# Kernel tuning notes

Measured on AMD Instinct MI355X. Metric: run time of the kernel, lower is better.

Reference implementation:

```python
import jax, jax.numpy as jnp
import numpy as np

PRIMES = [250007, 250013, 250027, 250031, 250037, 250043, 250049, 250051]
OFFSETS = np.concatenate([[0], np.cumsum(PRIMES)[:-1]]).astype(np.int64)  # [8]
TOTAL_ROWS = int(np.sum(PRIMES))
D_HEAD = 128          # embedding_dim_per_head
E_DIM = 8 * D_HEAD    # total_embedding_dim = 1024
H_DIM = 2560          # hidden_dim
KSIZE = 4             # causal depthwise conv kernel
EPS = 1e-6


def rmsnorm(x, g):
    # torch.nn.RMSNorm: x / sqrt(mean(x^2) + eps) * weight
    return x * jax.lax.rsqrt(jnp.mean(x * x, axis=-1, keepdims=True) + EPS) * g


def setup_inputs() -> dict:
    key = jax.random.key(0)
    ks = jax.random.split(key, 10)
    B, L = 4, 4096
    return {
        "hidden_states": jax.random.normal(ks[0], (B, L, H_DIM), jnp.float32),
        "engram_hash_indices": jax.random.randint(ks[1], (B, L, 8), 0, 250007, jnp.int64),
        "emb_table": jax.random.normal(ks[2], (TOTAL_ROWS, D_HEAD), jnp.float32) * 0.02,
        "w_v": jax.random.normal(ks[3], (H_DIM, E_DIM), jnp.float32) * 0.02,
        "w_k": jax.random.normal(ks[4], (H_DIM, E_DIM), jnp.float32) * 0.02,
        "g_h": jnp.ones((H_DIM,), jnp.float32),
        "g_k": jnp.ones((H_DIM,), jnp.float32),
        "g_v": jnp.ones((H_DIM,), jnp.float32),
        # paper zero-inits the conv; use small random weights so the conv path is exercised
        "conv_w": jax.random.normal(ks[5], (H_DIM, KSIZE), jnp.float32) * 0.02,
        "conv_b": jax.random.normal(ks[6], (H_DIM,), jnp.float32) * 0.02,
    }


def reference(hidden_states, engram_hash_indices, emb_table, w_v, w_k, g_h, g_k, g_v, conv_w, conv_b):
    B, L, H = hidden_states.shape
    # multi-head hash embedding retrieval
    idx = engram_hash_indices + jnp.asarray(OFFSETS)            # [B,L,8]
    e_t = emb_table[idx].reshape(B, L, E_DIM)                    # gather + concat heads
    # value / key projections (Linear, no bias)
    v_t = jnp.einsum('ble,he->blh', e_t, w_v)                    # [B,L,H]
    k_t = jnp.einsum('ble,he->blh', e_t, w_k)
    # context-aware gating
    h_n = rmsnorm(hidden_states, g_h)
    k_n = rmsnorm(k_t, g_k)
    dot = jnp.sum(h_n * k_n, axis=-1) / jnp.sqrt(jnp.float32(H))  # [B,L]
    stable = jnp.sqrt(jnp.maximum(jnp.abs(dot), 1e-6)) * jnp.sign(dot)
    alpha = jax.nn.sigmoid(stable)                               # [B,L]
    v_tilde = alpha[..., None] * v_t                             # [B,L,H]
    v_n = rmsnorm(v_tilde, g_v)
    # causal depthwise conv1d (left pad K-1) + SiLU
    x_pad = jnp.pad(v_n, ((0, 0), (KSIZE - 1, 0), (0, 0)))       # [B,L+3,H]
    conv = sum(conv_w[:, j] * x_pad[:, j:j + L, :] for j in range(KSIZE)) + conv_b
    y = jax.nn.silu(conv) + v_tilde
    return hidden_states + y
```

## Files before the change

kernel.cpp:

```cpp
#include <hip/hip_runtime.h>
#include <cstddef>
#include <cstdint>

typedef __bf16 bf16;
typedef __bf16 bf16x4 __attribute__((ext_vector_type(4)));
typedef __bf16 bf16x8 __attribute__((ext_vector_type(8)));
typedef float f32x4 __attribute__((ext_vector_type(4)));

#define AS1C(p) ((const __attribute__((address_space(1))) void*)(p))
#define AS3(p)  ((__attribute__((address_space(3))) void*)(p))

#define MROWS 16384
#define HDIM 2560
#define EDIM 1024
#define LSEQ 4096

static __device__ const int kHeadOff[8] = {0, 250007, 500020, 750047,
                                           1000078, 1250115, 1500158, 1750207};

__global__ __launch_bounds__(256) void k_gather(const int* __restrict__ hidx,
                                                const float* __restrict__ emb,
                                                bf16* __restrict__ E) {
  const int t = threadIdx.x;
  const int m = blockIdx.x * 2 + (t >> 7);
  const int tt = t & 127;
  const int head = tt >> 4;
  const int e8 = (tt & 15) * 8;
  const int rid = hidx[m * 8 + head] + kHeadOff[head];
  const float4 v0 = *(const float4*)(emb + (size_t)rid * 128 + e8);
  const float4 v1 = *(const float4*)(emb + (size_t)rid * 128 + e8 + 4);
  bf16x8 o;
  o[0] = (bf16)v0.x; o[1] = (bf16)v0.y; o[2] = (bf16)v0.z; o[3] = (bf16)v0.w;
  o[4] = (bf16)v1.x; o[5] = (bf16)v1.y; o[6] = (bf16)v1.z; o[7] = (bf16)v1.w;
  *(bf16x8*)(E + (size_t)m * EDIM + head * 128 + e8) = o;
}

__global__ __launch_bounds__(256) void k_cvt2(const float* __restrict__ s0,
                                              bf16* __restrict__ d0,
                                              const float* __restrict__ s1,
                                              bf16* __restrict__ d1) {
  int b = blockIdx.x;
  const float* src = s0;
  bf16* dst = d0;
  if (b >= 1280) { b -= 1280; src = s1; dst = d1; }
  const int i = (b * 256 + threadIdx.x) * 8;
  float4 a = *(const float4*)(src + i);
  float4 c = *(const float4*)(src + i + 4);
  bf16x8 o;
  o[0] = (bf16)a.x; o[1] = (bf16)a.y; o[2] = (bf16)a.z; o[3] = (bf16)a.w;
  o[4] = (bf16)c.x; o[5] = (bf16)c.y; o[6] = (bf16)c.z; o[7] = (bf16)c.w;
  *(bf16x8*)(dst + i) = o;
}

__device__ __forceinline__ float red16(float v) {
  v += __shfl_xor(v, 1);
  v += __shfl_xor(v, 2);
  v += __shfl_xor(v, 4);
  v += __shfl_xor(v, 8);
  return v;
}


#define LDSB 24576

__global__ __launch_bounds__(512, 4) void k_gemm(const bf16* __restrict__ A,
                                                 const bf16* __restrict__ Wv,
                                                 const bf16* __restrict__ Wk,
                                                 const float* __restrict__ hidden,
                                                 const float* __restrict__ g_h,
                                                 const float* __restrict__ g_k,
                                                 bf16* __restrict__ Vt,
                                                 float* __restrict__ S) {
  __shared__ __attribute__((aligned(16))) char ldsc[2 * LDSB];
  const int tid = threadIdx.x;
  const int wid = tid >> 6, lane = tid & 63;
  const int wm = wid >> 1, wn = wid & 1;
  const int r16 = lane & 15, khalf = lane >> 4;

  const int w = blockIdx.x;
  const int xcd = w & 7;
  const int r_ = w >> 3;
  const int gx = r_ >> 3;
  const int y = xcd * 8 + (r_ & 7);
  const int m0 = y * 256;
  const bool isV = (gx < 20);
  const int n0 = (isV ? gx : gx - 20) * 128;
  const bf16* Wp = isV ? Wv : Wk;

  const int sw = ((r16 >> 1) & 3) << 4;
  const int c0 = (khalf * 16) ^ sw;
  const int aRd = (wm * 64 + r16) * 64 + c0;
  const int bRd = 16384 + (wn * 64 + r16) * 64 + c0;

  const int srow = tid >> 2;
  const int scol = (((tid & 3) ^ ((tid >> 3) & 3))) * 8;
  const bf16* pA0 = A + (size_t)(m0 + srow) * EDIM + scol;
  const bf16* pA1 = pA0 + (size_t)128 * EDIM;
  const bf16* pB = Wp + (size_t)(n0 + srow) * EDIM + scol;
  const int ldsW = wid * 1024;

  f32x4 acc[4][4] = {};

#define STAGE(BUFO, KT) do {                                                   \
    __builtin_amdgcn_global_load_lds(AS1C(pA0 + (KT) * 32),                    \
        AS3(ldsc + (BUFO) + ldsW), 16, 0, 0);                                  \
    __builtin_amdgcn_global_load_lds(AS1C(pA1 + (KT) * 32),                    \
        AS3(ldsc + (BUFO) + 8192 + ldsW), 16, 0, 0);                           \
    __builtin_amdgcn_global_load_lds(AS1C(pB + (KT) * 32),                     \
        AS3(ldsc + (BUFO) + 16384 + ldsW), 16, 0, 0);                          \
    __builtin_amdgcn_sched_barrier(0);                                         \
  } while (0)

#define PHASE_CORE(BUFO) do {                                                  \
    bf16x8 aF[4], bF[4];                                                       \
    _Pragma("unroll") for (int mi = 0; mi < 4; ++mi)                           \
      aF[mi] = *(const bf16x8*)(ldsc + (BUFO) + aRd + mi * 1024);              \
    _Pragma("unroll") for (int nj = 0; nj < 4; ++nj)                           \
      bF[nj] = *(const bf16x8*)(ldsc + (BUFO) + bRd + nj * 1024);              \
    __builtin_amdgcn_s_setprio(1);                                             \
    _Pragma("unroll") for (int nj = 0; nj < 4; ++nj)                           \
      _Pragma("unroll") for (int mi = 0; mi < 4; ++mi)                         \
        acc[mi][nj] = __builtin_amdgcn_mfma_f32_16x16x32_bf16(                 \
            aF[mi], bF[nj], acc[mi][nj], 0, 0, 0);                             \
    __builtin_amdgcn_s_setprio(0);                                             \
    asm volatile("s_waitcnt lgkmcnt(0)" ::: "memory");                         \
    __builtin_amdgcn_s_barrier();                                              \
  } while (0)

#define BEGIN_PHASE3() do {                                                    \
    asm volatile("s_waitcnt vmcnt(3)" ::: "memory");                           \
    __builtin_amdgcn_s_barrier();                                              \
    asm volatile("" ::: "memory");                                             \
  } while (0)

#define BEGIN_PHASE0() do {                                                    \
    asm volatile("s_waitcnt vmcnt(0)" ::: "memory");                           \
    __builtin_amdgcn_s_barrier();                                              \
    asm volatile("" ::: "memory");                                             \
  } while (0)

  STAGE(0, 0);
  STAGE(LDSB, 1);

  for (int p = 0; p < 30; p += 2) {
    BEGIN_PHASE3();
    PHASE_CORE(0);
    STAGE(0, p + 2);
    BEGIN_PHASE3();
    PHASE_CORE(LDSB);
    STAGE(LDSB, p + 3);
  }
  BEGIN_PHASE3();
  PHASE_CORE(0);
  BEGIN_PHASE0();
  PHASE_CORE(LDSB);

  float* P = (float*)ldsc;
  if (isV) {
#pragma unroll
    for (int mi = 0; mi < 4; ++mi) {
#pragma unroll
      for (int nj = 0; nj < 4; ++nj) {
        const int col = n0 + wn * 64 + nj * 16 + r16;
#pragma unroll
        for (int r = 0; r < 4; ++r) {
          const int row = m0 + wm * 64 + mi * 16 + khalf * 4 + r;
          Vt[(size_t)row * HDIM + col] = (bf16)acc[mi][nj][r];
        }
      }
#pragma unroll
      for (int r = 0; r < 4; ++r) {
        float p = 0.f;
#pragma unroll
        for (int nj = 0; nj < 4; ++nj) p += acc[mi][nj][r] * acc[mi][nj][r];
        p = red16(p);
        if (r16 == 0) {
          const int rl = wm * 64 + mi * 16 + khalf * 4 + r;
          P[wn * 256 + rl] = p;
        }
      }
    }
    __syncthreads();
    if (tid < 256) {
      const float s = P[tid] + P[256 + tid];
      atomicAdd(&S[(size_t)(m0 + tid) * 4 + 3], s);
    }
  } else {
    float ghk[4];
#pragma unroll
    for (int nj = 0; nj < 4; ++nj) {
      const int col = n0 + wn * 64 + nj * 16 + r16;
      ghk[nj] = g_h[col] * g_k[col];
    }
#pragma unroll
    for (int mi = 0; mi < 4; ++mi) {
#pragma unroll
      for (int r = 0; r < 4; ++r) {
        const int row = m0 + wm * 64 + mi * 16 + khalf * 4 + r;
        float p1 = 0.f, p2 = 0.f, p3 = 0.f;
#pragma unroll
        for (int nj = 0; nj < 4; ++nj) {
          const int col = n0 + wn * 64 + nj * 16 + r16;
          const float k = acc[mi][nj][r];
          const float h = hidden[(size_t)row * HDIM + col];
          p1 += h * h;
          p2 += h * ghk[nj] * k;
          p3 += k * k;
        }
        p1 = red16(p1); p2 = red16(p2); p3 = red16(p3);
        if (r16 == 0) {
          const int rl = wm * 64 + mi * 16 + khalf * 4 + r;
          float* Pr = P + (wn * 256 + rl) * 3;
          Pr[0] = p1; Pr[1] = p2; Pr[2] = p3;
        }
      }
    }
    __syncthreads();
    for (int j = tid; j < 768; j += 512) {
      const int rl = j / 3, c = j % 3;
      const float s = P[j] + P[768 + j];
      atomicAdd(&S[(size_t)(m0 + rl) * 4 + c], s);
    }
  }
#undef STAGE
#undef PHASE_CORE
#undef BEGIN_PHASE3
#undef BEGIN_PHASE0
}

__global__ __launch_bounds__(256) void k_scal(const float* __restrict__ S,
                                              float* __restrict__ AB) {
  const int m = blockIdx.x * 256 + threadIdx.x;
  const float s1 = S[(size_t)m * 4 + 0];
  const float s2 = S[(size_t)m * 4 + 1];
  const float s3 = S[(size_t)m * 4 + 2];
  const float s4 = S[(size_t)m * 4 + 3];
  const float inv_h = rsqrtf(s1 * (1.f / HDIM) + 1e-6f);
  const float inv_k = rsqrtf(s3 * (1.f / HDIM) + 1e-6f);
  const float dot = s2 * inv_h * inv_k * 0.019764235f;
  float st = sqrtf(fmaxf(fabsf(dot), 1e-6f));
  st = (dot < 0.f) ? -st : st;
  if (dot == 0.f) st = 0.f;
  const float alpha = 1.f / (1.f + __expf(-st));
  const float inv_v = rsqrtf(alpha * alpha * s4 * (1.f / HDIM) + 1e-6f);
  AB[(size_t)m * 2 + 0] = alpha;
  AB[(size_t)m * 2 + 1] = alpha * inv_v;
}

__global__ __launch_bounds__(320) void k_fuse(const float* __restrict__ hidden,
                                              const bf16* __restrict__ Vt,
                                              const float* __restrict__ AB,
                                              const float* __restrict__ g_v,
                                              const float* __restrict__ conv_w,
                                              const float* __restrict__ conv_b,
                                              float* __restrict__ out) {
  const int mbase = blockIdx.x * 8;
  const int l0 = mbase & (LSEQ - 1);
  const int t = threadIdx.x;
  const int h0 = t * 8;

  float gv[8], cb[8];
  *(float4*)&gv[0] = *(const float4*)(g_v + h0);
  *(float4*)&gv[4] = *(const float4*)(g_v + h0 + 4);
  *(float4*)&cb[0] = *(const float4*)(conv_b + h0);
  *(float4*)&cb[4] = *(const float4*)(conv_b + h0 + 4);
  float4 cw[8];
#pragma unroll
  for (int i = 0; i < 8; ++i)
    cw[i] = *(const float4*)(conv_w + (size_t)(h0 + i) * 4);

  float win[4][8];
#pragma unroll
  for (int jj = 0; jj < 4; ++jj)
#pragma unroll
    for (int i = 0; i < 8; ++i) win[jj][i] = 0.f;

#pragma unroll
  for (int j = 0; j < 11; ++j) {
    const int lj = l0 - 3 + j;
    const int m = mbase - 3 + j;
    float vtl[8];
    if (lj >= 0) {
      const float alpha = AB[(size_t)m * 2 + 0];
      const float av = AB[(size_t)m * 2 + 1];
      const bf16x8 v = *(const bf16x8*)(Vt + (size_t)m * HDIM + h0);
#pragma unroll
      for (int i = 0; i < 8; ++i) {
        const float vt = (float)v[i];
        vtl[i] = alpha * vt;
        win[j & 3][i] = av * vt * gv[i];
      }
    } else {
#pragma unroll
      for (int i = 0; i < 8; ++i) { win[j & 3][i] = 0.f; vtl[i] = 0.f; }
    }
    if (j >= 3) {
      const int R = mbase + j - 3;
      const size_t base = (size_t)R * HDIM + h0;
      float hx[8];
      *(float4*)&hx[0] = *(const float4*)(hidden + base);
      *(float4*)&hx[4] = *(const float4*)(hidden + base + 4);
      float o[8];
#pragma unroll
      for (int i = 0; i < 8; ++i) {
        float c = cb[i];
        c += ((const float*)&cw[i])[0] * win[(j - 3) & 3][i];
        c += ((const float*)&cw[i])[1] * win[(j - 2) & 3][i];
        c += ((const float*)&cw[i])[2] * win[(j - 1) & 3][i];
        c += ((const float*)&cw[i])[3] * win[j & 3][i];
        const float y = c / (1.f + __expf(-c));
        o[i] = hx[i] + y + vtl[i];
      }
      *(float4*)(out + base) = *(float4*)&o[0];
      *(float4*)(out + base + 4) = *(float4*)&o[4];
    }
  }
}

extern "C" void kernel_launch(void* const* d_in, const int* in_sizes, int n_in,
                              void* d_out, int out_size, void* d_ws,
                              size_t ws_size, hipStream_t stream) {
  const float* hidden = (const float*)d_in[0];
  const int* hashidx = (const int*)d_in[1];
  const float* emb = (const float*)d_in[2];
  const float* w_v = (const float*)d_in[3];
  const float* w_k = (const float*)d_in[4];
  const float* g_h = (const float*)d_in[5];
  const float* g_k = (const float*)d_in[6];
  const float* g_v = (const float*)d_in[7];
  const float* conv_w = (const float*)d_in[8];
  const float* conv_b = (const float*)d_in[9];
  float* out = (float*)d_out;

  char* w = (char*)d_ws;
  bf16* e16 = (bf16*)w;  w += (size_t)MROWS * EDIM * 2;
  bf16* wv16 = (bf16*)w; w += (size_t)HDIM * EDIM * 2;
  bf16* wk16 = (bf16*)w; w += (size_t)HDIM * EDIM * 2;
  bf16* vt16 = (bf16*)w; w += (size_t)MROWS * HDIM * 2;
  float* S = (float*)w;  w += (size_t)MROWS * 4 * 4;
  float* AB = (float*)w; w += (size_t)MROWS * 2 * 4;

  hipMemsetAsync(S, 0, (size_t)MROWS * 4 * 4, stream);
  k_gather<<<MROWS / 2, 256, 0, stream>>>(hashidx, emb, e16);
  k_cvt2<<<2560, 256, 0, stream>>>(w_v, wv16, w_k, wk16);
  k_gemm<<<dim3(2560), 512, 0, stream>>>(e16, wv16, wk16, hidden, g_h, g_k,
                                         vt16, S);
  k_scal<<<MROWS / 256, 256, 0, stream>>>(S, AB);
  k_fuse<<<MROWS / 8, 320, 0, stream>>>(hidden, vt16, AB, g_v, conv_w, conv_b,
                                        out);
}
```

Baseline: 325.4 us.

## Pre-pack gathered A in MFMA fragment layout and load A directly into registers

The gather kernel now writes the bf16 embedding matrix in a pre-swizzled fragment-major layout, so each lane of a GEMM wave can read its MFMA A-operand with one contiguous 16-byte global load. The GEMM stops staging A through LDS: it double-buffers A fragments in registers (aX/aY) and only stages the weight tile B through LDS, which cuts LDS use from 48KB to 16KB and removes the A LDS writes and reads. The cost is A reuse across the two wn waves, which now comes from L2/cache instead of LDS, and extra register pressure. The gather kernel also changes its thread mapping, with each thread now converting a 64-element half-row per head.

Result: slower. 335.8 us (+3.2%).

```diff
diff --git a/kernel.cpp b/kernel.cpp
--- a/kernel.cpp
+++ b/kernel.cpp
@@ -20,19 +20,26 @@
 
 __global__ __launch_bounds__(256) void k_gather(const int* __restrict__ hidx,
                                                 const float* __restrict__ emb,
-                                                bf16* __restrict__ E) {
+                                                bf16* __restrict__ Ap) {
   const int t = threadIdx.x;
-  const int m = blockIdx.x * 2 + (t >> 7);
-  const int tt = t & 127;
-  const int head = tt >> 4;
-  const int e8 = (tt & 15) * 8;
-  const int rid = hidx[m * 8 + head] + kHeadOff[head];
-  const float4 v0 = *(const float4*)(emb + (size_t)rid * 128 + e8);
-  const float4 v1 = *(const float4*)(emb + (size_t)rid * 128 + e8 + 4);
-  bf16x8 o;
-  o[0] = (bf16)v0.x; o[1] = (bf16)v0.y; o[2] = (bf16)v0.z; o[3] = (bf16)v0.w;
-  o[4] = (bf16)v1.x; o[5] = (bf16)v1.y; o[6] = (bf16)v1.z; o[7] = (bf16)v1.w;
-  *(bf16x8*)(E + (size_t)m * EDIM + head * 128 + e8) = o;
+  const int m16 = t & 15, c = t >> 4;
+  const int mbase = blockIdx.x * 16;
+  const int head = c >> 1;
+  const int rid = hidx[(mbase + m16) * 8 + head] + kHeadOff[head];
+  const float* src = emb + (size_t)rid * 128 + (c & 1) * 64;
+  char* dstbase = (char*)Ap + ((size_t)blockIdx.x * 32 + c * 2) * 1024;
+#pragma unroll
+  for (int j64 = 0; j64 < 2; ++j64) {
+#pragma unroll
+    for (int q = 0; q < 4; ++q) {
+      const float4 v0 = *(const float4*)(src + j64 * 32 + q * 8);
+      const float4 v1 = *(const float4*)(src + j64 * 32 + q * 8 + 4);
+      bf16x8 o;
+      o[0] = (bf16)v0.x; o[1] = (bf16)v0.y; o[2] = (bf16)v0.z; o[3] = (bf16)v0.w;
+      o[4] = (bf16)v1.x; o[5] = (bf16)v1.y; o[6] = (bf16)v1.z; o[7] = (bf16)v1.w;
+      *(bf16x8*)(dstbase + j64 * 1024 + (m16 + 16 * q) * 16) = o;
+    }
+  }
 }
 
 __global__ __launch_bounds__(256) void k_cvt2(const float* __restrict__ s0,
@@ -61,9 +68,7 @@
 }
 
 
-#define LDSB 24576
-
-__global__ __launch_bounds__(512, 4) void k_gemm(const bf16* __restrict__ A,
+__global__ __launch_bounds__(512, 4) void k_gemm(const bf16* __restrict__ Af,
                                                  const bf16* __restrict__ Wv,
                                                  const bf16* __restrict__ Wk,
                                                  const float* __restrict__ hidden,
@@ -71,7 +76,7 @@
                                                  const float* __restrict__ g_k,
                                                  bf16* __restrict__ Vt,
                                                  float* __restrict__ S) {
-  __shared__ __attribute__((aligned(16))) char ldsc[2 * LDSB];
+  __shared__ __attribute__((aligned(16))) char ldsc[16384];
   const int tid = threadIdx.x;
   const int wid = tid >> 6, lane = tid & 63;
   const int wm = wid >> 1, wn = wid & 1;
@@ -87,73 +92,58 @@
   const int n0 = (isV ? gx : gx - 20) * 128;
   const bf16* Wp = isV ? Wv : Wk;
 
+  const char* aF0 = (const char*)Af + ((size_t)(y * 16 + wm * 4) * 32) * 1024 +
+                    lane * 16;
   const int sw = ((r16 >> 1) & 3) << 4;
   const int c0 = (khalf * 16) ^ sw;
-  const int aRd = (wm * 64 + r16) * 64 + c0;
-  const int bRd = 16384 + (wn * 64 + r16) * 64 + c0;
+  const int bRd = (wn * 64 + r16) * 64 + c0;
 
   const int srow = tid >> 2;
   const int scol = (((tid & 3) ^ ((tid >> 3) & 3))) * 8;
-  const bf16* pA0 = A + (size_t)(m0 + srow) * EDIM + scol;
-  const bf16* pA1 = pA0 + (size_t)128 * EDIM;
   const bf16* pB = Wp + (size_t)(n0 + srow) * EDIM + scol;
-  const int ldsW = wid * 1024;
 
   f32x4 acc[4][4] = {};
-
-#define STAGE(BUFO, KT) do {                                                   \
-    __builtin_amdgcn_global_load_lds(AS1C(pA0 + (KT) * 32),                    \
-        AS3(ldsc + (BUFO) + ldsW), 16, 0, 0);                                  \
-    __builtin_amdgcn_global_load_lds(AS1C(pA1 + (KT) * 32),                    \
-        AS3(ldsc + (BUFO) + 8192 + ldsW), 16, 0, 0);                           \
+  bf16x8 aX[4], aY[4], bF[4];
+
+#define STAGEB(BUFO, KT) do {                                                  \
     __builtin_amdgcn_global_load_lds(AS1C(pB + (KT) * 32),                     \
-        AS3(ldsc + (BUFO) + 16384 + ldsW), 16, 0, 0);                          \
+        AS3(ldsc + (BUFO) + tid * 16), 16, 0, 0);                              \
     __builtin_amdgcn_sched_barrier(0);                                         \
   } while (0)
 
-#define PHASE_CORE(BUFO) do {                                                  \
-    bf16x8 aF[4], bF[4];                                                       \
+#define LOADA(DST, KT) do {                                                    \
     _Pragma("unroll") for (int mi = 0; mi < 4; ++mi)                           \
-      aF[mi] = *(const bf16x8*)(ldsc + (BUFO) + aRd + mi * 1024);              \
+      DST[mi] = *(const bf16x8*)(aF0 + ((size_t)mi * 32 + (KT)) * 1024);       \
+  } while (0)
+
+#define PHASE(BUFO, ACUR, ANEXT, KT, LD_A, ST_B, VMC) do {                     \
+    asm volatile("s_waitcnt vmcnt(" #VMC ")" ::: "memory");                    \
+    __builtin_amdgcn_s_barrier();                                              \
+    asm volatile("" ::: "memory");                                             \
+    if (LD_A) LOADA(ANEXT, (KT) + 1);                                          \
     _Pragma("unroll") for (int nj = 0; nj < 4; ++nj)                           \
       bF[nj] = *(const bf16x8*)(ldsc + (BUFO) + bRd + nj * 1024);              \
     __builtin_amdgcn_s_setprio(1);                                             \
     _Pragma("unroll") for (int nj = 0; nj < 4; ++nj)                           \
       _Pragma("unroll") for (int mi = 0; mi < 4; ++mi)                         \
         acc[mi][nj] = __builtin_amdgcn_mfma_f32_16x16x32_bf16(                 \
-            aF[mi], bF[nj], acc[mi][nj], 0, 0, 0);                             \
+            ACUR[mi], bF[nj], acc[mi][nj], 0, 0, 0);                           \
     __builtin_amdgcn_s_setprio(0);                                             \
     asm volatile("s_waitcnt lgkmcnt(0)" ::: "memory");                         \
     __builtin_amdgcn_s_barrier();                                              \
+    if (ST_B) STAGEB(BUFO, (KT) + 2);                                          \
   } while (0)
 
-#define BEGIN_PHASE3() do {                                                    \
-    asm volatile("s_waitcnt vmcnt(3)" ::: "memory");                           \
-    __builtin_amdgcn_s_barrier();                                              \
-    asm volatile("" ::: "memory");                                             \
-  } while (0)
-
-#define BEGIN_PHASE0() do {                                                    \
-    asm volatile("s_waitcnt vmcnt(0)" ::: "memory");                           \
-    __builtin_amdgcn_s_barrier();                                              \
-    asm volatile("" ::: "memory");                                             \
-  } while (0)
-
-  STAGE(0, 0);
-  STAGE(LDSB, 1);
+  STAGEB(0, 0);
+  STAGEB(8192, 1);
+  LOADA(aX, 0);
 
   for (int p = 0; p < 30; p += 2) {
-    BEGIN_PHASE3();
-    PHASE_CORE(0);
-    STAGE(0, p + 2);
-    BEGIN_PHASE3();
-    PHASE_CORE(LDSB);
-    STAGE(LDSB, p + 3);
+    PHASE(0, aX, aY, p, true, true, 5);
+    PHASE(8192, aY, aX, p + 1, true, true, 5);
   }
-  BEGIN_PHASE3();
-  PHASE_CORE(0);
-  BEGIN_PHASE0();
-  PHASE_CORE(LDSB);
+  PHASE(0, aX, aY, 30, true, false, 5);
+  PHASE(8192, aY, aX, 31, false, false, 4);
 
   float* P = (float*)ldsc;
   if (isV) {
@@ -222,10 +212,9 @@
       atomicAdd(&S[(size_t)(m0 + rl) * 4 + c], s);
     }
   }
-#undef STAGE
-#undef PHASE_CORE
-#undef BEGIN_PHASE3
-#undef BEGIN_PHASE0
+#undef STAGEB
+#undef LOADA
+#undef PHASE
 }
 
 __global__ __launch_bounds__(256) void k_scal(const float* __restrict__ S,
@@ -333,7 +322,7 @@
   float* out = (float*)d_out;
 
   char* w = (char*)d_ws;
-  bf16* e16 = (bf16*)w;  w += (size_t)MROWS * EDIM * 2;
+  bf16* a16 = (bf16*)w;  w += (size_t)MROWS * EDIM * 2;
   bf16* wv16 = (bf16*)w; w += (size_t)HDIM * EDIM * 2;
   bf16* wk16 = (bf16*)w; w += (size_t)HDIM * EDIM * 2;
   bf16* vt16 = (bf16*)w; w += (size_t)MROWS * HDIM * 2;
@@ -341,9 +330,9 @@
   float* AB = (float*)w; w += (size_t)MROWS * 2 * 4;
 
   hipMemsetAsync(S, 0, (size_t)MROWS * 4 * 4, stream);
-  k_gather<<<MROWS / 2, 256, 0, stream>>>(hashidx, emb, e16);
+  k_gather<<<MROWS / 16, 256, 0, stream>>>(hashidx, emb, a16);
   k_cvt2<<<2560, 256, 0, stream>>>(w_v, wv16, w_k, wk16);
-  k_gemm<<<dim3(2560), 512, 0, stream>>>(e16, wv16, wk16, hidden, g_h, g_k,
+  k_gemm<<<dim3(2560), 512, 0, stream>>>(a16, wv16, wk16, hidden, g_h, g_k,
                                          vt16, S);
   k_scal<<<MROWS / 256, 256, 0, stream>>>(S, AB);
   k_fuse<<<MROWS / 8, 320, 0, stream>>>(hidden, vt16, AB, g_v, conv_w, conv_b,
```

## Triple-buffer GEMM LDS pipeline and fold scalar kernel into fuse kernel

Applied to the files above, without the earlier changes.

The GEMM main loop moves from double to triple buffering in LDS, issuing the next tile's global-to-LDS loads at the start of each phase. The goal is to cut the stall between the barrier and the next load. Separately, the per-row gating scalars (alpha and the value-norm scale) are now computed inline in the fuse kernel from S, which removes the k_scal launch and the AB buffer. The cost is larger LDS use (72KB per block), which may reduce occupancy, and redundant per-row scalar math in each fuse thread.

New measurement: 329.7 us. No clear change (+1.3%).

```diff
diff --git a/kernel.cpp b/kernel.cpp
--- a/kernel.cpp
+++ b/kernel.cpp
@@ -71,7 +71,7 @@
                                                  const float* __restrict__ g_k,
                                                  bf16* __restrict__ Vt,
                                                  float* __restrict__ S) {
-  __shared__ __attribute__((aligned(16))) char ldsc[2 * LDSB];
+  __shared__ __attribute__((aligned(16))) char ldsc[3 * LDSB];
   const int tid = threadIdx.x;
   const int wid = tid >> 6, lane = tid & 63;
   const int wm = wid >> 1, wn = wid & 1;
@@ -111,7 +111,8 @@
     __builtin_amdgcn_sched_barrier(0);                                         \
   } while (0)
 
-#define PHASE_CORE(BUFO) do {                                                  \
+#define PHASE(BUFO, STBUF, KT, ST, VMW) do {                                   \
+    if (ST) STAGE(STBUF, (KT) + 2);                                            \
     bf16x8 aF[4], bF[4];                                                       \
     _Pragma("unroll") for (int mi = 0; mi < 4; ++mi)                           \
       aF[mi] = *(const bf16x8*)(ldsc + (BUFO) + aRd + mi * 1024);              \
@@ -123,37 +124,22 @@
         acc[mi][nj] = __builtin_amdgcn_mfma_f32_16x16x32_bf16(                 \
             aF[mi], bF[nj], acc[mi][nj], 0, 0, 0);                             \
     __builtin_amdgcn_s_setprio(0);                                             \
-    asm volatile("s_waitcnt lgkmcnt(0)" ::: "memory");                         \
+    asm volatile("s_waitcnt " VMW " lgkmcnt(0)" ::: "memory");                 \
     __builtin_amdgcn_s_barrier();                                              \
   } while (0)
 
-#define BEGIN_PHASE3() do {                                                    \
-    asm volatile("s_waitcnt vmcnt(3)" ::: "memory");                           \
-    __builtin_amdgcn_s_barrier();                                              \
-    asm volatile("" ::: "memory");                                             \
-  } while (0)
-
-#define BEGIN_PHASE0() do {                                                    \
-    asm volatile("s_waitcnt vmcnt(0)" ::: "memory");                           \
-    __builtin_amdgcn_s_barrier();                                              \
-    asm volatile("" ::: "memory");                                             \
-  } while (0)
-
   STAGE(0, 0);
   STAGE(LDSB, 1);
-
-  for (int p = 0; p < 30; p += 2) {
-    BEGIN_PHASE3();
-    PHASE_CORE(0);
-    STAGE(0, p + 2);
-    BEGIN_PHASE3();
-    PHASE_CORE(LDSB);
-    STAGE(LDSB, p + 3);
+  asm volatile("s_waitcnt vmcnt(3)" ::: "memory");
+  __builtin_amdgcn_s_barrier();
+
+  for (int p = 0; p < 30; p += 3) {
+    PHASE(0,        2 * LDSB, p,     true, "vmcnt(3)");
+    PHASE(LDSB,     0,        p + 1, true, "vmcnt(3)");
+    PHASE(2 * LDSB, LDSB,     p + 2, true, "vmcnt(3)");
   }
-  BEGIN_PHASE3();
-  PHASE_CORE(0);
-  BEGIN_PHASE0();
-  PHASE_CORE(LDSB);
+  PHASE(0, 0, 30, false, "vmcnt(0)");
+  PHASE(LDSB, 0, 31, false, "");
 
   float* P = (float*)ldsc;
   if (isV) {
@@ -223,33 +209,25 @@
     }
   }
 #undef STAGE
-#undef PHASE_CORE
-#undef BEGIN_PHASE3
-#undef BEGIN_PHASE0
-}
-
-__global__ __launch_bounds__(256) void k_scal(const float* __restrict__ S,
-                                              float* __restrict__ AB) {
-  const int m = blockIdx.x * 256 + threadIdx.x;
-  const float s1 = S[(size_t)m * 4 + 0];
-  const float s2 = S[(size_t)m * 4 + 1];
-  const float s3 = S[(size_t)m * 4 + 2];
-  const float s4 = S[(size_t)m * 4 + 3];
-  const float inv_h = rsqrtf(s1 * (1.f / HDIM) + 1e-6f);
-  const float inv_k = rsqrtf(s3 * (1.f / HDIM) + 1e-6f);
-  const float dot = s2 * inv_h * inv_k * 0.019764235f;
+#undef PHASE
+}
+
+__device__ __forceinline__ void row_scal(const float* __restrict__ S, int m,
+                                         float& alpha, float& av) {
+  const float4 s = *(const float4*)(S + (size_t)m * 4);
+  const float inv_h = rsqrtf(s.x * (1.f / HDIM) + 1e-6f);
+  const float inv_k = rsqrtf(s.z * (1.f / HDIM) + 1e-6f);
+  const float dot = s.y * inv_h * inv_k * 0.019764235f;
   float st = sqrtf(fmaxf(fabsf(dot), 1e-6f));
   st = (dot < 0.f) ? -st : st;
   if (dot == 0.f) st = 0.f;
-  const float alpha = 1.f / (1.f + __expf(-st));
-  const float inv_v = rsqrtf(alpha * alpha * s4 * (1.f / HDIM) + 1e-6f);
-  AB[(size_t)m * 2 + 0] = alpha;
-  AB[(size_t)m * 2 + 1] = alpha * inv_v;
+  alpha = 1.f / (1.f + __expf(-st));
+  av = alpha * rsqrtf(alpha * alpha * s.w * (1.f / HDIM) + 1e-6f);
 }
 
 __global__ __launch_bounds__(320) void k_fuse(const float* __restrict__ hidden,
                                               const bf16* __restrict__ Vt,
-                                              const float* __restrict__ AB,
+                                              const float* __restrict__ S,
                                               const float* __restrict__ g_v,
                                               const float* __restrict__ conv_w,
                                               const float* __restrict__ conv_b,
@@ -281,8 +259,8 @@
     const int m = mbase - 3 + j;
     float vtl[8];
     if (lj >= 0) {
-      const float alpha = AB[(size_t)m * 2 + 0];
-      const float av = AB[(size_t)m * 2 + 1];
+      float alpha, av;
+      row_scal(S, m, alpha, av);
       const bf16x8 v = *(const bf16x8*)(Vt + (size_t)m * HDIM + h0);
 #pragma unroll
       for (int i = 0; i < 8; ++i) {
@@ -338,14 +316,12 @@
   bf16* wk16 = (bf16*)w; w += (size_t)HDIM * EDIM * 2;
   bf16* vt16 = (bf16*)w; w += (size_t)MROWS * HDIM * 2;
   float* S = (float*)w;  w += (size_t)MROWS * 4 * 4;
-  float* AB = (float*)w; w += (size_t)MROWS * 2 * 4;
 
   hipMemsetAsync(S, 0, (size_t)MROWS * 4 * 4, stream);
   k_gather<<<MROWS / 2, 256, 0, stream>>>(hashidx, emb, e16);
   k_cvt2<<<2560, 256, 0, stream>>>(w_v, wv16, w_k, wk16);
   k_gemm<<<dim3(2560), 512, 0, stream>>>(e16, wv16, wk16, hidden, g_h, g_k,
                                          vt16, S);
-  k_scal<<<MROWS / 256, 256, 0, stream>>>(S, AB);
-  k_fuse<<<MROWS / 8, 320, 0, stream>>>(hidden, vt16, AB, g_v, conv_w, conv_b,
+  k_fuse<<<MROWS / 8, 320, 0, stream>>>(hidden, vt16, S, g_v, conv_w, conv_b,
                                         out);
 }
```
